# Kernel optimization log

Measured on AMD Instinct MI355X. Metric: run time of the kernel, lower is better.

## Reference

```python
import jax, jax.numpy as jnp
import numpy as np

TEMPERATURE = 30.0


def _adaptive_pool_28(sk):
    # sk: [b, 1, H, W] with H, W divisible by 28 -> [b, 1, 28, 28]
    b, c, h, w = sk.shape
    fh, fw = h // 28, w // 28
    return sk.reshape(b, c, 28, fh, 28, fw).mean(axis=(3, 5))


def setup_inputs() -> dict:
    key = jax.random.key(0)
    ks = jax.random.split(key, 6)
    bs, C, H, W, K = 8, 256, 64, 64, 16
    return {
        "x": jax.random.normal(ks[0], (bs, C, H, W), dtype=jnp.float32),
        "scene_knowledge": jax.random.normal(ks[1], (bs, 1, 56, 56), dtype=jnp.float32),
        "weight": jax.random.normal(ks[2], (K, C, C, 3, 3), dtype=jnp.float32) * 0.02,
        "bias": jax.random.normal(ks[3], (K, C), dtype=jnp.float32) * 0.02,
        "att_w1": jax.random.normal(ks[4], (196, 784), dtype=jnp.float32) * 0.05,
        "att_w2": jax.random.normal(ks[5], (16, 196), dtype=jnp.float32) * 0.05,
    }


def reference(x, scene_knowledge, weight, bias, att_w1, att_w2):
    bs, C, h, w = x.shape
    K = weight.shape[0]

    # ---- Attention: pooled scene knowledge -> softmax over K experts ----
    pooled = _adaptive_pool_28(scene_knowledge).reshape(bs, 28 * 28)  # [bs, 784]
    hdn = jax.nn.relu(pooled @ att_w1.T)                               # [bs, 196]
    logits = hdn @ att_w2.T                                            # [bs, K]
    att = jax.nn.softmax(logits / TEMPERATURE, axis=-1)                # [bs, K]

    # ---- Aggregate per-sample conv weights and biases ----
    agg_w = jnp.einsum("bk,koihw->boihw", att, weight)  # [bs, C, C, 3, 3]
    agg_b = att @ bias                                   # [bs, C]

    # ---- Per-sample conv (equivalent to groups=bs trick in torch) ----
    def per_sample_conv(xi, wi):
        # xi: [C, h, w], wi: [C, C, 3, 3]
        return jax.lax.conv_general_dilated(
            xi[None], wi, window_strides=(1, 1), padding="SAME",
            dimension_numbers=("NCHW", "OIHW", "NCHW"))[0]

    out = jax.vmap(per_sample_conv)(x, agg_w)            # [bs, C, h, w]
    out = out + agg_b[:, :, None, None] + x              # bias + residual
    return out
```

## Files before the change

### kernel.cpp

```cpp
#include <hip/hip_runtime.h>
#include <stdint.h>
#include <stddef.h>

typedef __bf16 bf16;
typedef __bf16 bf16x8 __attribute__((ext_vector_type(8)));
typedef __bf16 bf16x4 __attribute__((ext_vector_type(4)));
typedef __bf16 bf16x2 __attribute__((ext_vector_type(2)));
typedef float f32x4 __attribute__((ext_vector_type(4)));

static_assert(sizeof(bf16x8) == 16, "bf16x8 must be 16B");

__device__ __forceinline__ void gload_lds16(const void* g, void* l) {
    __builtin_amdgcn_global_load_lds(
        (const __attribute__((address_space(1))) uint32_t*)g,
        (__attribute__((address_space(3))) uint32_t*)l, 16, 0, 0);
}

__global__ __launch_bounds__(1024) void attn_kernel(const float* __restrict__ sk,
                                                    const float* __restrict__ w1,
                                                    const float* __restrict__ w2,
                                                    float* __restrict__ att) {
    const int b = blockIdx.x, t = threadIdx.x;
    __shared__ float pooled[784];
    __shared__ float hdn[196];
    __shared__ float logits[16];
    const float* skb = sk + (size_t)b * 3136;
    if (t < 784) {
        int oy = t / 28, ox = t % 28;
        const float* p = skb + (oy * 2) * 56 + ox * 2;
        pooled[t] = 0.25f * (p[0] + p[1] + p[56] + p[57]);
    }
    __syncthreads();
    const int q = t & 15, jg = t >> 4;
#pragma unroll
    for (int rep = 0; rep < 4; ++rep) {
        const int j = rep * 64 + jg;
        float s = 0.f;
        if (j < 196) {
            const float* wr = w1 + (size_t)j * 784 + q;
#pragma unroll 7
            for (int i = 0; i < 49; ++i) s += pooled[q + i * 16] * wr[i * 16];
        }
#pragma unroll
        for (int off = 8; off; off >>= 1) s += __shfl_xor(s, off, 16);
        if (j < 196 && q == 0) hdn[j] = s > 0.f ? s : 0.f;
    }
    __syncthreads();
    if (t < 256) {
        const int jj = t >> 4, qq = t & 15;
        float s = 0.f;
#pragma unroll
        for (int i = 0; i < 13; ++i) {
            const int idx = qq + i * 16;
            if (idx < 196) s += hdn[idx] * w2[jj * 196 + idx];
        }
#pragma unroll
        for (int off = 8; off; off >>= 1) s += __shfl_xor(s, off, 16);
        if (qq == 0) logits[jj] = s * (1.0f / 30.0f);
    }
    __syncthreads();
    if (t == 0) {
        float m = logits[0];
        for (int k = 1; k < 16; ++k) m = fmaxf(m, logits[k]);
        float e16[16], sum = 0.f;
        for (int k = 0; k < 16; ++k) { e16[k] = expf(logits[k] - m); sum += e16[k]; }
        float inv = 1.f / sum;
        for (int k = 0; k < 16; ++k) att[b * 16 + k] = e16[k] * inv;
    }
}

__global__ __launch_bounds__(256) void aggt_kernel(
    const float* __restrict__ weight,
    const float* __restrict__ bias,
    const float* __restrict__ att,
    bf16* __restrict__ aggw,
    float* __restrict__ aggb,
    const float* __restrict__ x,
    bf16* __restrict__ xt) {
    __shared__ __align__(16) char smem[73984];
    const int t = threadIdx.x;

    if (blockIdx.x >= 128) {
        const int bid = blockIdx.x - 128;
        const int b = bid >> 6, y = bid & 63;
        bf16* T = (bf16*)smem;
        const float* src = x + (size_t)b * 256 * 4096 + (size_t)y * 64;
        for (int i = 0; i < 16; ++i) {
            int v = t + 256 * i;
            int ci = v >> 4, x4 = (v & 15) * 4;
            float4 f = *(const float4*)(src + (size_t)ci * 4096 + x4);
            bf16* d = &T[ci * 64 + x4];
            d[0] = (bf16)f.x; d[1] = (bf16)f.y; d[2] = (bf16)f.z; d[3] = (bf16)f.w;
        }
        __syncthreads();
        bf16* dstb = xt + (size_t)bid * 16384;
        for (int i = 0; i < 8; ++i) {
            int c2 = t + 256 * i;
            int cg = c2 >> 6, xx = c2 & 63;
            bf16x8 v;
#pragma unroll
            for (int c = 0; c < 8; ++c) v[c] = T[(cg * 8 + c) * 64 + xx];
            *(bf16x8*)(dstb + (size_t)c2 * 8) = v;
        }
        return;
    }

    const int chunk = blockIdx.x >> 5, cog = blockIdx.x & 31;
    const int half = cog >> 4;
    bf16* accW = (bf16*)smem;

    if (chunk == 0 && t < 64) {
        const int b = t >> 3, co = cog * 8 + (t & 7);
        float s = 0.f;
        for (int k = 0; k < 16; ++k) s += att[b * 16 + k] * bias[k * 256 + co];
        aggb[b * 256 + co] = s;
    }

#pragma unroll
    for (int r = 0; r < 9; ++r) {
        const int id = t + 256 * r;
        const int co_i = id / 288, e2 = id - co_i * 288;
        const int co = cog * 8 + co_i;
        const float* wbase = weight + (size_t)co * 2304 + (size_t)chunk * 576 + 2 * e2;
        float2 wv[16];
#pragma unroll
        for (int k = 0; k < 16; ++k)
            wv[k] = *(const float2*)(wbase + (size_t)k * 589824);
        float a[8][2];
#pragma unroll
        for (int b = 0; b < 8; ++b) { a[b][0] = 0.f; a[b][1] = 0.f; }
#pragma unroll
        for (int k = 0; k < 16; ++k) {
#pragma unroll
            for (int b = 0; b < 8; ++b) {
                const float av = att[b * 16 + k];
                a[b][0] += av * wv[k].x;
                a[b][1] += av * wv[k].y;
            }
        }
#pragma unroll
        for (int b = 0; b < 8; ++b) {
            bf16x2 v; v[0] = (bf16)a[b][0]; v[1] = (bf16)a[b][1];
            *(bf16x2*)&accW[(co_i * 8 + b) * 578 + 2 * e2] = v;
        }
    }
    __syncthreads();

    const int cogl = cog & 15;
#pragma unroll
    for (int i = 0; i < 18; ++i) {
        const int s = t + 256 * i;
        const int piece = s >> 3, sub = s & 7;
        const int b = piece / 72, r = piece - b * 72;
        const int pos = r >> 3, cg = r & 7;
        bf16x8 v;
#pragma unroll
        for (int c = 0; c < 8; ++c)
            v[c] = accW[(sub * 8 + b) * 578 + (cg * 8 + c) * 9 + pos];
        const size_t G = ((((size_t)b * 9 + pos) * 4 + chunk) * 2 + half) * 8 + cg;
        *(bf16x8*)(aggw + G * 1024 + cogl * 64 + sub * 8) = v;
    }
}

__global__ __launch_bounds__(256, 2) void conv_kernel(
    const bf16* __restrict__ xt, const bf16* __restrict__ aggw,
    const float* __restrict__ aggb, const float* __restrict__ xin,
    float* __restrict__ out) {
    const int bid = blockIdx.x;
    const int slice = bid & 15, ytile = bid >> 4;
    const int b = slice >> 1, half = slice & 1;
    const int tid = threadIdx.x;
    const int wave = tid >> 6, lane = tid & 63;
    const int wm = wave & 1, wn = wave >> 1;
    const int lane15 = lane & 15, quad = lane >> 4;

    __shared__ __align__(16) bf16 Xs[4][8][66][8];
    __shared__ __align__(16) bf16 Ws[8][128][8];

    f32x4 acc[4][4];
#pragma unroll
    for (int mt = 0; mt < 4; ++mt)
#pragma unroll
        for (int nt = 0; nt < 4; ++nt) acc[mt][nt] = f32x4{0.f, 0.f, 0.f, 0.f};

    {
        uint4 z; z.x = z.y = z.z = z.w = 0u;
        uint4* p = (uint4*)&Xs[0][0][0][0];
        for (int i = tid; i < 2112; i += 256) p[i] = z;
    }

    const int yrow = ytile * 2 - 1 + wave;
    const bool rowok = (yrow >= 0) && (yrow < 64);
    const bf16* xsrc = xt + ((size_t)b * 64 + (rowok ? yrow : 0)) * 16384 + (size_t)lane * 8;
    bf16* xdstbase = &Xs[wave][0][1][0];

    for (int chunk = 0; chunk < 4; ++chunk) {
        __syncthreads();
        if (rowok) {
            const bf16* s0 = xsrc + (size_t)chunk * 4096;
#pragma unroll
            for (int cg = 0; cg < 8; ++cg)
                gload_lds16(s0 + cg * 512, xdstbase + cg * 528);
        }
        const bf16* wchunkbase = aggw + (((size_t)b * 36 + chunk) * 2 + half) * 8192;
        for (int pos = 0; pos < 9; ++pos) {
            if (pos) __syncthreads();
            const bf16* wsrc = wchunkbase + (size_t)pos * 65536 + wave * 2048 + (size_t)lane * 8;
            bf16* wdst = ((bf16*)Ws) + wave * 2048;
#pragma unroll
            for (int i = 0; i < 4; ++i)
                gload_lds16(wsrc + i * 512, wdst + i * 512);
            __syncthreads();
            const int kh = pos / 3, kw = pos - kh * 3;
            const int xr = wn + kh;
#pragma unroll
            for (int s = 0; s < 2; ++s) {
                const int cg = s * 4 + quad;
                bf16x8 afr[4], bfr[4];
#pragma unroll
                for (int mt = 0; mt < 4; ++mt)
                    afr[mt] = *(const bf16x8*)&Ws[cg][wm * 64 + mt * 16 + lane15][0];
#pragma unroll
                for (int nt = 0; nt < 4; ++nt)
                    bfr[nt] = *(const bf16x8*)&Xs[xr][cg][kw + nt * 16 + lane15][0];
#pragma unroll
                for (int mt = 0; mt < 4; ++mt)
#pragma unroll
                    for (int nt = 0; nt < 4; ++nt)
                        acc[mt][nt] = __builtin_amdgcn_mfma_f32_16x16x32_bf16(
                            afr[mt], bfr[nt], acc[mt][nt], 0, 0, 0);
            }
        }
    }

    const int y = ytile * 2 + wn;
#pragma unroll
    for (int mt = 0; mt < 4; ++mt) {
#pragma unroll
        for (int r = 0; r < 4; ++r) {
            const int co = half * 128 + wm * 64 + mt * 16 + quad * 4 + r;
            const float bbv = aggb[b * 256 + co];
            const size_t rowbase = (((size_t)b * 256 + co) * 64 + y) * 64;
#pragma unroll
            for (int nt = 0; nt < 4; ++nt) {
                const size_t oidx = rowbase + nt * 16 + lane15;
                out[oidx] = acc[mt][nt][r] + bbv + xin[oidx];
            }
        }
    }
}

extern "C" void kernel_launch(void* const* d_in, const int* in_sizes, int n_in,
                              void* d_out, int out_size, void* d_ws, size_t ws_size,
                              hipStream_t stream) {
    const float* x    = (const float*)d_in[0];
    const float* sk   = (const float*)d_in[1];
    const float* wgt  = (const float*)d_in[2];
    const float* bias = (const float*)d_in[3];
    const float* w1   = (const float*)d_in[4];
    const float* w2   = (const float*)d_in[5];
    float* out = (float*)d_out;

    char* ws = (char*)d_ws;
    float* att  = (float*)(ws + 0);
    float* aggb = (float*)(ws + 1024);
    bf16*  aggw = (bf16*)(ws + 16384);
    bf16*  xt   = (bf16*)(ws + 16384 + 9437184);

    attn_kernel<<<8, 1024, 0, stream>>>(sk, w1, w2, att);
    aggt_kernel<<<640, 256, 0, stream>>>(wgt, bias, att, aggw, aggb, x, xt);
    conv_kernel<<<512, 256, 0, stream>>>(xt, aggw, aggb, x, out);
}
```

Before: 178.8 us.

## Fuse attention computation into aggregation kernel, recomputing per block

Removes the separate attention kernel and has each weight-aggregation block recompute the pooled scene features, the two-layer MLP and the softmax for all 8 samples into shared memory. This eliminates one kernel launch and the global round trip for the attention vector. In exchange, every aggregation block redundantly reads w1 and does the MLP before starting its weight loads, which adds latency to each block.

```diff
diff --git a/kernel.cpp b/kernel.cpp
--- a/kernel.cpp
+++ b/kernel.cpp
@@ -16,63 +16,12 @@
         (__attribute__((address_space(3))) uint32_t*)l, 16, 0, 0);
 }
 
-__global__ __launch_bounds__(1024) void attn_kernel(const float* __restrict__ sk,
-                                                    const float* __restrict__ w1,
-                                                    const float* __restrict__ w2,
-                                                    float* __restrict__ att) {
-    const int b = blockIdx.x, t = threadIdx.x;
-    __shared__ float pooled[784];
-    __shared__ float hdn[196];
-    __shared__ float logits[16];
-    const float* skb = sk + (size_t)b * 3136;
-    if (t < 784) {
-        int oy = t / 28, ox = t % 28;
-        const float* p = skb + (oy * 2) * 56 + ox * 2;
-        pooled[t] = 0.25f * (p[0] + p[1] + p[56] + p[57]);
-    }
-    __syncthreads();
-    const int q = t & 15, jg = t >> 4;
-#pragma unroll
-    for (int rep = 0; rep < 4; ++rep) {
-        const int j = rep * 64 + jg;
-        float s = 0.f;
-        if (j < 196) {
-            const float* wr = w1 + (size_t)j * 784 + q;
-#pragma unroll 7
-            for (int i = 0; i < 49; ++i) s += pooled[q + i * 16] * wr[i * 16];
-        }
-#pragma unroll
-        for (int off = 8; off; off >>= 1) s += __shfl_xor(s, off, 16);
-        if (j < 196 && q == 0) hdn[j] = s > 0.f ? s : 0.f;
-    }
-    __syncthreads();
-    if (t < 256) {
-        const int jj = t >> 4, qq = t & 15;
-        float s = 0.f;
-#pragma unroll
-        for (int i = 0; i < 13; ++i) {
-            const int idx = qq + i * 16;
-            if (idx < 196) s += hdn[idx] * w2[jj * 196 + idx];
-        }
-#pragma unroll
-        for (int off = 8; off; off >>= 1) s += __shfl_xor(s, off, 16);
-        if (qq == 0) logits[jj] = s * (1.0f / 30.0f);
-    }
-    __syncthreads();
-    if (t == 0) {
-        float m = logits[0];
-        for (int k = 1; k < 16; ++k) m = fmaxf(m, logits[k]);
-        float e16[16], sum = 0.f;
-        for (int k = 0; k < 16; ++k) { e16[k] = expf(logits[k] - m); sum += e16[k]; }
-        float inv = 1.f / sum;
-        for (int k = 0; k < 16; ++k) att[b * 16 + k] = e16[k] * inv;
-    }
-}
-
 __global__ __launch_bounds__(256) void aggt_kernel(
     const float* __restrict__ weight,
     const float* __restrict__ bias,
-    const float* __restrict__ att,
+    const float* __restrict__ sk,
+    const float* __restrict__ w1,
+    const float* __restrict__ w2,
     bf16* __restrict__ aggw,
     float* __restrict__ aggb,
     const float* __restrict__ x,
@@ -107,12 +56,67 @@
 
     const int chunk = blockIdx.x >> 5, cog = blockIdx.x & 31;
     const int half = cog >> 4;
+
+    float* pooled_s = (float*)smem;
+    float* hdn_s = (float*)(smem + 25088);
+    __shared__ float att_s[8][16];
+
+#pragma unroll
+    for (int b = 0; b < 8; ++b) {
+        const float* skb = sk + (size_t)b * 3136;
+        for (int e = t; e < 784; e += 256) {
+            int oy = e / 28, ox = e % 28;
+            const float* p = skb + (oy * 2) * 56 + ox * 2;
+            pooled_s[b * 784 + e] = 0.25f * (p[0] + p[1] + p[56] + p[57]);
+        }
+    }
+    __syncthreads();
+    {
+        const int q = t & 15, g = t >> 4;
+        for (int j = g; j < 196; j += 16) {
+            float s[8];
+#pragma unroll
+            for (int b = 0; b < 8; ++b) s[b] = 0.f;
+            const float* wr = w1 + (size_t)j * 784 + q;
+            for (int i = 0; i < 49; ++i) {
+                const float wv = wr[i * 16];
+                const int idx = q + i * 16;
+#pragma unroll
+                for (int b = 0; b < 8; ++b) s[b] += pooled_s[b * 784 + idx] * wv;
+            }
+#pragma unroll
+            for (int off = 8; off; off >>= 1)
+#pragma unroll
+                for (int b = 0; b < 8; ++b) s[b] += __shfl_xor(s[b], off, 16);
+            if (q == 0)
+#pragma unroll
+                for (int b = 0; b < 8; ++b) hdn_s[b * 196 + j] = s[b] > 0.f ? s[b] : 0.f;
+        }
+    }
+    __syncthreads();
+    if (t < 128) {
+        const int b = t >> 4, k = t & 15;
+        float s = 0.f;
+        const float* wr = w2 + (size_t)k * 196;
+        for (int j = 0; j < 196; ++j) s += hdn_s[b * 196 + j] * wr[j];
+        float l = s * (1.0f / 30.0f);
+        float m = l;
+#pragma unroll
+        for (int off = 8; off; off >>= 1) m = fmaxf(m, __shfl_xor(m, off, 16));
+        float e = expf(l - m);
+        float sum = e;
+#pragma unroll
+        for (int off = 8; off; off >>= 1) sum += __shfl_xor(sum, off, 16);
+        att_s[b][k] = e / sum;
+    }
+    __syncthreads();
+
     bf16* accW = (bf16*)smem;
 
     if (chunk == 0 && t < 64) {
         const int b = t >> 3, co = cog * 8 + (t & 7);
         float s = 0.f;
-        for (int k = 0; k < 16; ++k) s += att[b * 16 + k] * bias[k * 256 + co];
+        for (int k = 0; k < 16; ++k) s += att_s[b][k] * bias[k * 256 + co];
         aggb[b * 256 + co] = s;
     }
 
@@ -133,7 +137,7 @@
         for (int k = 0; k < 16; ++k) {
 #pragma unroll
             for (int b = 0; b < 8; ++b) {
-                const float av = att[b * 16 + k];
+                const float av = att_s[b][k];
                 a[b][0] += av * wv[k].x;
                 a[b][1] += av * wv[k].y;
             }
@@ -262,12 +266,10 @@
     float* out = (float*)d_out;
 
     char* ws = (char*)d_ws;
-    float* att  = (float*)(ws + 0);
     float* aggb = (float*)(ws + 1024);
     bf16*  aggw = (bf16*)(ws + 16384);
     bf16*  xt   = (bf16*)(ws + 16384 + 9437184);
 
-    attn_kernel<<<8, 1024, 0, stream>>>(sk, w1, w2, att);
-    aggt_kernel<<<640, 256, 0, stream>>>(wgt, bias, att, aggw, aggb, x, xt);
+    aggt_kernel<<<640, 256, 0, stream>>>(wgt, bias, sk, w1, w2, aggw, aggb, x, xt);
     conv_kernel<<<512, 256, 0, stream>>>(xt, aggw, aggb, x, out);
 }
```

After: 247.5 us. 38.4% more time.

## Split weight-aggregation blocks finer and use wave-wide reductions in attention

Applied to the files above, without the earlier changes.

The weight aggregation work is split across twice as many blocks, each handling half of a 64-input-channel chunk, which halves shared memory per block and allows four blocks per CU. The attention hidden layer now uses one full wave per output row with coalesced loads of w1 and a 64-lane shuffle reduction, replacing the 16-lane groups with strided loads. This aims to raise occupancy and memory parallelism in the bandwidth-bound aggregation, at the cost of more blocks, some idle threads in the last iteration, and more index arithmetic.

```diff
diff --git a/kernel.cpp b/kernel.cpp
--- a/kernel.cpp
+++ b/kernel.cpp
@@ -31,19 +31,18 @@
         pooled[t] = 0.25f * (p[0] + p[1] + p[56] + p[57]);
     }
     __syncthreads();
-    const int q = t & 15, jg = t >> 4;
-#pragma unroll
-    for (int rep = 0; rep < 4; ++rep) {
-        const int j = rep * 64 + jg;
-        float s = 0.f;
-        if (j < 196) {
-            const float* wr = w1 + (size_t)j * 784 + q;
-#pragma unroll 7
-            for (int i = 0; i < 49; ++i) s += pooled[q + i * 16] * wr[i * 16];
-        }
-#pragma unroll
-        for (int off = 8; off; off >>= 1) s += __shfl_xor(s, off, 16);
-        if (j < 196 && q == 0) hdn[j] = s > 0.f ? s : 0.f;
+    {
+        const int wv = t >> 6, ln = t & 63;
+        for (int j = wv; j < 196; j += 16) {
+            const float* wr = w1 + (size_t)j * 784;
+            float s = 0.f;
+#pragma unroll
+            for (int i = 0; i < 12; ++i) s += pooled[ln + 64 * i] * wr[ln + 64 * i];
+            if (ln < 16) s += pooled[768 + ln] * wr[768 + ln];
+#pragma unroll
+            for (int off = 32; off; off >>= 1) s += __shfl_xor(s, off, 64);
+            if (ln == 0) hdn[j] = s > 0.f ? s : 0.f;
+        }
     }
     __syncthreads();
     if (t < 256) {
@@ -69,7 +68,7 @@
     }
 }
 
-__global__ __launch_bounds__(256) void aggt_kernel(
+__global__ __launch_bounds__(256, 4) void aggt_kernel(
     const float* __restrict__ weight,
     const float* __restrict__ bias,
     const float* __restrict__ att,
@@ -77,11 +76,11 @@
     float* __restrict__ aggb,
     const float* __restrict__ x,
     bf16* __restrict__ xt) {
-    __shared__ __align__(16) char smem[73984];
+    __shared__ __align__(16) char smem[37120];
     const int t = threadIdx.x;
 
-    if (blockIdx.x >= 128) {
-        const int bid = blockIdx.x - 128;
+    if (blockIdx.x >= 256) {
+        const int bid = blockIdx.x - 256;
         const int b = bid >> 6, y = bid & 63;
         bf16* T = (bf16*)smem;
         const float* src = x + (size_t)b * 256 * 4096 + (size_t)y * 64;
@@ -105,59 +104,62 @@
         return;
     }
 
-    const int chunk = blockIdx.x >> 5, cog = blockIdx.x & 31;
-    const int half = cog >> 4;
+    const int chunkq = blockIdx.x >> 5, cog = blockIdx.x & 31;
+    const int chunk = chunkq >> 1, cghalf = chunkq & 1;
+    const int half = cog >> 4, cogl = cog & 15;
     bf16* accW = (bf16*)smem;
 
-    if (chunk == 0 && t < 64) {
+    if (chunkq == 0 && t < 64) {
         const int b = t >> 3, co = cog * 8 + (t & 7);
         float s = 0.f;
         for (int k = 0; k < 16; ++k) s += att[b * 16 + k] * bias[k * 256 + co];
         aggb[b * 256 + co] = s;
     }
 
-#pragma unroll
-    for (int r = 0; r < 9; ++r) {
+    for (int r = 0; r < 5; ++r) {
         const int id = t + 256 * r;
-        const int co_i = id / 288, e2 = id - co_i * 288;
-        const int co = cog * 8 + co_i;
-        const float* wbase = weight + (size_t)co * 2304 + (size_t)chunk * 576 + 2 * e2;
-        float2 wv[16];
-#pragma unroll
-        for (int k = 0; k < 16; ++k)
-            wv[k] = *(const float2*)(wbase + (size_t)k * 589824);
-        float a[8][2];
-#pragma unroll
-        for (int b = 0; b < 8; ++b) { a[b][0] = 0.f; a[b][1] = 0.f; }
-#pragma unroll
-        for (int k = 0; k < 16; ++k) {
+        if (id < 1152) {
+            const int co_i = id / 144, e2 = id - co_i * 144;
+            const int co = cog * 8 + co_i;
+            const float* wbase = weight + (size_t)co * 2304 + (size_t)chunk * 576
+                               + cghalf * 288 + 2 * e2;
+            float2 wv[16];
+#pragma unroll
+            for (int k = 0; k < 16; ++k)
+                wv[k] = *(const float2*)(wbase + (size_t)k * 589824);
+            float a[8][2];
+#pragma unroll
+            for (int b = 0; b < 8; ++b) { a[b][0] = 0.f; a[b][1] = 0.f; }
+#pragma unroll
+            for (int k = 0; k < 16; ++k) {
+#pragma unroll
+                for (int b = 0; b < 8; ++b) {
+                    const float av = att[b * 16 + k];
+                    a[b][0] += av * wv[k].x;
+                    a[b][1] += av * wv[k].y;
+                }
+            }
 #pragma unroll
             for (int b = 0; b < 8; ++b) {
-                const float av = att[b * 16 + k];
-                a[b][0] += av * wv[k].x;
-                a[b][1] += av * wv[k].y;
-            }
-        }
-#pragma unroll
-        for (int b = 0; b < 8; ++b) {
-            bf16x2 v; v[0] = (bf16)a[b][0]; v[1] = (bf16)a[b][1];
-            *(bf16x2*)&accW[(co_i * 8 + b) * 578 + 2 * e2] = v;
-        }
-    }
-    __syncthreads();
-
-    const int cogl = cog & 15;
-#pragma unroll
-    for (int i = 0; i < 18; ++i) {
+                bf16x2 v; v[0] = (bf16)a[b][0]; v[1] = (bf16)a[b][1];
+                *(bf16x2*)&accW[(co_i * 8 + b) * 290 + 2 * e2] = v;
+            }
+        }
+    }
+    __syncthreads();
+
+#pragma unroll
+    for (int i = 0; i < 9; ++i) {
         const int s = t + 256 * i;
         const int piece = s >> 3, sub = s & 7;
-        const int b = piece / 72, r = piece - b * 72;
-        const int pos = r >> 3, cg = r & 7;
+        const int b = piece / 36, r2 = piece - b * 36;
+        const int pos = r2 >> 2, cg_loc = r2 & 3;
         bf16x8 v;
 #pragma unroll
         for (int c = 0; c < 8; ++c)
-            v[c] = accW[(sub * 8 + b) * 578 + (cg * 8 + c) * 9 + pos];
-        const size_t G = ((((size_t)b * 9 + pos) * 4 + chunk) * 2 + half) * 8 + cg;
+            v[c] = accW[(sub * 8 + b) * 290 + (cg_loc * 8 + c) * 9 + pos];
+        const size_t G = ((((size_t)b * 9 + pos) * 4 + chunk) * 2 + half) * 8
+                       + cghalf * 4 + cg_loc;
         *(bf16x8*)(aggw + G * 1024 + cogl * 64 + sub * 8) = v;
     }
 }
@@ -268,6 +270,6 @@
     bf16*  xt   = (bf16*)(ws + 16384 + 9437184);
 
     attn_kernel<<<8, 1024, 0, stream>>>(sk, w1, w2, att);
-    aggt_kernel<<<640, 256, 0, stream>>>(wgt, bias, att, aggw, aggb, x, xt);
+    aggt_kernel<<<768, 256, 0, stream>>>(wgt, bias, att, aggw, aggb, x, xt);
     conv_kernel<<<512, 256, 0, stream>>>(xt, aggw, aggb, x, out);
 }
```

Measured after the change: 171.6 us. 1.04x faster.
